# Optimization experiments

Hardware: AMD Instinct MI355X
Metric: run time of the kernel (lower is better)

## Reference

```python
import jax, jax.numpy as jnp
import numpy as np

B, D, K = 8192, 2048, 2048  # batch, input dim, output_dim (must be equal: k==d required by call())


def setup_inputs() -> dict:
    key = jax.random.key(0)
    k1, k2, k3, k4 = jax.random.split(key, 4)
    lim_w = float(np.sqrt(6.0 / (K + D)))        # glorot_uniform for W (k,d)
    lim_v = float(np.sqrt(6.0 / (2 * D + K)))    # glorot_uniform for V (2d,k)
    return {
        "e1": jax.random.normal(k1, (B, D), jnp.float32),
        "e2": jax.random.normal(k2, (B, D), jnp.float32),
        "W": jax.random.uniform(k3, (K, D), jnp.float32, -lim_w, lim_w),
        "V": jax.random.uniform(k4, (2 * D, K), jnp.float32, -lim_v, lim_v),
        "b": jnp.zeros((K,), jnp.float32),
    }


def reference(e1, e2, W, V, b):
    # Faithful translation of the active call() of NeuralTensorDiagLayer.
    # call() tiles flatten(e1) k times and reshapes to (B, d, k); index algebra
    # shows x[p, q, r] = e1[(p*d+q)%B, r] * e2[(p*d+q)%B, r] * W[q, r]
    # (requires k == d for the W broadcast), then mean over the last axis (size k).
    # Equivalent efficient form: u = ((e1*e2) @ W.T)/k, then gather rows (p*d+q)%B.
    bsz, d = e1.shape
    k = W.shape[0]
    ff = jnp.concatenate([e1, e2], axis=-1) @ V              # (B, k) feedforward GEMM
    u = ((e1 * e2) @ W.T) / k                                # (B, k) diag bilinear, mean over k
    cols = jnp.arange(k)[None, :]                            # (1, k)
    rows = (jnp.arange(bsz)[:, None] * d + cols) % bsz       # (B, k) batch-mixing index from tile/reshape
    z = u[rows, cols]                                        # (B, k)
    return jnp.tanh(z + ff + b)
```

## Files before the change

kernel.cpp:

```cpp
#include <hip/hip_runtime.h>
#include <hip/hip_bf16.h>

typedef __bf16 bf16;
typedef bf16 bf16x8 __attribute__((ext_vector_type(8)));
typedef bf16 bf16x4 __attribute__((ext_vector_type(4)));
typedef float f32x4 __attribute__((ext_vector_type(4)));

#define AS1 __attribute__((address_space(1)))
#define AS3 __attribute__((address_space(3)))

__device__ __forceinline__ void gload_lds16(const void* g, void* l) {
    __builtin_amdgcn_global_load_lds((const AS1 void*)g, (AS3 void*)l, 16, 0, 0);
}

__device__ __forceinline__ float tanh_fast(float x) {
    float e = __expf(2.0f * x);
    return fmaf(-2.0f, __builtin_amdgcn_rcpf(e + 1.0f), 1.0f);
}

__global__ __launch_bounds__(256) void conv_fused(
    const float* __restrict__ e1, const float* __restrict__ e2,
    const float* __restrict__ W, const float* __restrict__ V,
    bf16* __restrict__ Xb, bf16* __restrict__ Vt, float* __restrict__ zs)
{
    __shared__ float tile[64][65];
    const int bid = blockIdx.x;
    const int t = threadIdx.x;

    if (bid < 8192) {
        const int r = bid;
        const int c = r & 2047, m = r >> 11;
        const size_t rb = (size_t)r * 2048;

        const float4* p1 = (const float4*)(e1 + rb) + t * 2;
        const float4* p2 = (const float4*)(e2 + rb) + t * 2;
        const float4* pw = (const float4*)(W + (size_t)c * 2048) + t * 2;
        float4 a0 = p1[0], a1 = p1[1];
        float4 b0 = p2[0], b1 = p2[1];
        float4 w0 = pw[0], w1 = pw[1];

        float dot = a0.x*b0.x*w0.x + a0.y*b0.y*w0.y + a0.z*b0.z*w0.z + a0.w*b0.w*w0.w
                  + a1.x*b1.x*w1.x + a1.y*b1.y*w1.y + a1.z*b1.z*w1.z + a1.w*b1.w*w1.w;

        bf16x8 xa, xb;
        xa[0]=(bf16)a0.x; xa[1]=(bf16)a0.y; xa[2]=(bf16)a0.z; xa[3]=(bf16)a0.w;
        xa[4]=(bf16)a1.x; xa[5]=(bf16)a1.y; xa[6]=(bf16)a1.z; xa[7]=(bf16)a1.w;
        xb[0]=(bf16)b0.x; xb[1]=(bf16)b0.y; xb[2]=(bf16)b0.z; xb[3]=(bf16)b0.w;
        xb[4]=(bf16)b1.x; xb[5]=(bf16)b1.y; xb[6]=(bf16)b1.z; xb[7]=(bf16)b1.w;

        *(bf16x8*)(Xb + (size_t)r * 4096 + t * 8)        = xa;
        *(bf16x8*)(Xb + (size_t)r * 4096 + 2048 + t * 8) = xb;

        #pragma unroll
        for (int off = 32; off; off >>= 1) dot += __shfl_xor(dot, off);
        float* red = &tile[0][0];
        if ((t & 63) == 0) red[t >> 6] = dot;
        __syncthreads();
        if (t == 0) zs[m * 2048 + c] = (red[0]+red[1]+red[2]+red[3]) * (1.0f/2048.0f);
    } else {
        const int vb = bid - 8192;
        const int k0 = (vb >> 5) * 64;
        const int c0 = (vb & 31) * 64;
        const int rr = t >> 4;
        const int cc = (t & 15) * 4;

        #pragma unroll
        for (int r4 = 0; r4 < 4; ++r4) {
            int row = r4 * 16 + rr;
            float4 v = *(const float4*)(V + (size_t)(k0 + row) * 2048 + c0 + cc);
            tile[row][cc + 0] = v.x; tile[row][cc + 1] = v.y;
            tile[row][cc + 2] = v.z; tile[row][cc + 3] = v.w;
        }
        __syncthreads();
        #pragma unroll
        for (int r4 = 0; r4 < 4; ++r4) {
            int crow = r4 * 16 + rr;
            bf16x4 o;
            o[0] = (bf16)tile[cc + 0][crow];
            o[1] = (bf16)tile[cc + 1][crow];
            o[2] = (bf16)tile[cc + 2][crow];
            o[3] = (bf16)tile[cc + 3][crow];
            *(bf16x4*)(Vt + (size_t)(c0 + crow) * 4096 + k0 + cc) = o;
        }
    }
}

__global__ __launch_bounds__(512, 2) void gemm_ep(
    const bf16* __restrict__ Xb, const bf16* __restrict__ Vt,
    const float* __restrict__ zs, const float* __restrict__ bias,
    float* __restrict__ out)
{
    extern __shared__ char smem[];
    const int tid  = threadIdx.x;
    const int lane = tid & 63;
    const int wid  = tid >> 6;
    const int wr = wid >> 2, wc = wid & 3;
    const int mtile = blockIdx.x & 31;
    const int ntile = blockIdx.x >> 5;
    const int row0 = mtile * 256, col0 = ntile * 256;

    const int srow = tid >> 3;
    const int scb  = ((tid & 7) * 16) ^ ((srow & 7) << 4);
    const bf16* Abase = Xb + (size_t)(row0 + srow) * 4096 + (scb >> 1);
    const bf16* Bbase = Vt + (size_t)(col0 + srow) * 4096 + (scb >> 1);

    const int lr  = lane & 15;
    const int lkb = (lane >> 4) * 16;

    f32x4 acc[2][2][4][2] = {};
    bf16x8 aA[4][2];
    bf16x8 bB[2][2][2];

    auto stage = [&](int c, int kt) {
        char* Al = smem + c * 65536 + tid * 16;
        char* Bl = smem + c * 65536 + 32768 + tid * 16;
        const bf16* Ag = Abase + (size_t)kt * 64;
        const bf16* Bg = Bbase + (size_t)kt * 64;
        #pragma unroll
        for (int r = 0; r < 4; ++r) gload_lds16(Ag + (size_t)r * 262144, Al + r * 8192);
        #pragma unroll
        for (int r = 0; r < 4; ++r) gload_lds16(Bg + (size_t)r * 262144, Bl + r * 8192);
    };

    auto ldsA = [&](const char* Ab, int qm, int i, int ks) -> bf16x8 {
        const int R = wr * 128 + qm * 64 + i * 16 + lr;
        const int cb = ks * 64 + lkb;
        return *(const bf16x8*)(Ab + R * 128 + (cb ^ ((R & 7) << 4)));
    };
    auto ldsB = [&](const char* Bb, int qn, int j, int ks) -> bf16x8 {
        const int R = wc * 64 + qn * 32 + j * 16 + lr;
        const int cb = ks * 64 + lkb;
        return *(const bf16x8*)(Bb + R * 128 + (cb ^ ((R & 7) << 4)));
    };

    auto window1 = [&](int c) {
        const char* Ab = smem + c * 65536;
        const char* Bb = smem + c * 65536 + 32768;
        #pragma unroll
        for (int i = 0; i < 4; ++i) { aA[i][0] = ldsA(Ab, 0, i, 0); aA[i][1] = ldsA(Ab, 0, i, 1); }
        #pragma unroll
        for (int j = 0; j < 2; ++j) { bB[0][j][0] = ldsB(Bb, 0, j, 0); bB[0][j][1] = ldsB(Bb, 0, j, 1); }
        __builtin_amdgcn_s_setprio(1);
        #pragma unroll
        for (int ks = 0; ks < 2; ++ks)
            #pragma unroll
            for (int i = 0; i < 4; ++i)
                #pragma unroll
                for (int j = 0; j < 2; ++j)
                    acc[0][0][i][j] = __builtin_amdgcn_mfma_f32_16x16x32_bf16(
                        aA[i][ks], bB[0][j][ks], acc[0][0][i][j], 0, 0, 0);
        __builtin_amdgcn_s_setprio(0);
        #pragma unroll
        for (int j = 0; j < 2; ++j) { bB[1][j][0] = ldsB(Bb, 1, j, 0); bB[1][j][1] = ldsB(Bb, 1, j, 1); }
        __builtin_amdgcn_s_setprio(1);
        #pragma unroll
        for (int ks = 0; ks < 2; ++ks)
            #pragma unroll
            for (int i = 0; i < 4; ++i)
                #pragma unroll
                for (int j = 0; j < 2; ++j)
                    acc[0][1][i][j] = __builtin_amdgcn_mfma_f32_16x16x32_bf16(
                        aA[i][ks], bB[1][j][ks], acc[0][1][i][j], 0, 0, 0);
        __builtin_amdgcn_s_setprio(0);
        #pragma unroll
        for (int i = 0; i < 4; ++i) { aA[i][0] = ldsA(Ab, 1, i, 0); aA[i][1] = ldsA(Ab, 1, i, 1); }
        __builtin_amdgcn_s_setprio(1);
        #pragma unroll
        for (int ks = 0; ks < 2; ++ks)
            #pragma unroll
            for (int i = 0; i < 4; ++i)
                #pragma unroll
                for (int j = 0; j < 2; ++j)
                    acc[1][1][i][j] = __builtin_amdgcn_mfma_f32_16x16x32_bf16(
                        aA[i][ks], bB[1][j][ks], acc[1][1][i][j], 0, 0, 0);
        __builtin_amdgcn_s_setprio(0);
    };

    auto mfma_q10 = [&]() {
        __builtin_amdgcn_s_setprio(1);
        #pragma unroll
        for (int ks = 0; ks < 2; ++ks)
            #pragma unroll
            for (int i = 0; i < 4; ++i)
                #pragma unroll
                for (int j = 0; j < 2; ++j)
                    acc[1][0][i][j] = __builtin_amdgcn_mfma_f32_16x16x32_bf16(
                        aA[i][ks], bB[0][j][ks], acc[1][0][i][j], 0, 0, 0);
        __builtin_amdgcn_s_setprio(0);
    };

    stage(0, 0);
    stage(1, 1);
    asm volatile("s_waitcnt vmcnt(8)" ::: "memory");
    __builtin_amdgcn_s_barrier();

    #pragma unroll 2
    for (int t = 0; t < 62; ++t) {
        const int c = t & 1;
        window1(c);
        __builtin_amdgcn_s_barrier();
        stage(c, t + 2);
        mfma_q10();
        asm volatile("s_waitcnt vmcnt(8)" ::: "memory");
        __builtin_amdgcn_s_barrier();
    }
    window1(0);
    __builtin_amdgcn_s_barrier();
    mfma_q10();
    asm volatile("s_waitcnt vmcnt(0)" ::: "memory");
    __builtin_amdgcn_s_barrier();
    window1(1);
    mfma_q10();

    const int lq = lane >> 4;
    float zb[2][2][4];
    #pragma unroll
    for (int qn = 0; qn < 2; ++qn)
        #pragma unroll
        for (int j = 0; j < 2; ++j) {
            const int ccol = col0 + wc * 64 + qn * 32 + j * 16 + lr;
            const float bb = bias[ccol];
            #pragma unroll
            for (int q = 0; q < 4; ++q) zb[qn][j][q] = zs[q * 2048 + ccol] + bb;
        }
    #pragma unroll
    for (int qm = 0; qm < 2; ++qm)
        #pragma unroll
        for (int i = 0; i < 4; ++i)
            #pragma unroll
            for (int q = 0; q < 4; ++q) {
                float* orow = out + (size_t)(row0 + wr * 128 + qm * 64 + i * 16
                                             + lq * 4 + q) * 2048
                                  + col0 + wc * 64 + lr;
                #pragma unroll
                for (int qn = 0; qn < 2; ++qn)
                    #pragma unroll
                    for (int j = 0; j < 2; ++j)
                        orow[qn * 32 + j * 16] =
                            tanh_fast(acc[qm][qn][i][j][q] + zb[qn][j][q]);
            }
}

extern "C" void kernel_launch(void* const* d_in, const int* in_sizes, int n_in,
                              void* d_out, int out_size, void* d_ws, size_t ws_size,
                              hipStream_t stream) {
    const float* e1 = (const float*)d_in[0];
    const float* e2 = (const float*)d_in[1];
    const float* W  = (const float*)d_in[2];
    const float* V  = (const float*)d_in[3];
    const float* b  = (const float*)d_in[4];
    float* out = (float*)d_out;

    char* ws = (char*)d_ws;
    bf16*  Xb = (bf16*)ws;
    bf16*  Vt = (bf16*)(ws + (size_t)64 * 1024 * 1024);
    float* zs = (float*)(ws + (size_t)80 * 1024 * 1024);

    conv_fused<<<10240, 256, 0, stream>>>(e1, e2, W, V, Xb, Vt, zs);

    hipFuncSetAttribute((const void*)gemm_ep,
                        hipFuncAttributeMaxDynamicSharedMemorySize, 131072);
    gemm_ep<<<256, 512, 131072, stream>>>(Xb, Vt, zs, b, out);
}
```

Baseline: 162.4 us.

## Fuse fp32-to-bf16 conversion of activations into the GEMM A-tile loader

The prep kernel no longer writes a bf16 copy of concat(e1,e2) to the workspace. The GEMM now loads fp32 e1/e2 tiles into registers, converts them to bf16 and writes them into swizzled LDS. B tiles still arrive through direct global-to-LDS loads. This removes a large intermediate write and re-read, but it doubles the bytes fetched per A tile, replaces async LDS loads with register-staged ones and adds register pressure under the 512-thread, 2-block launch bound.

```diff
diff --git a/kernel.cpp b/kernel.cpp
--- a/kernel.cpp
+++ b/kernel.cpp
@@ -21,7 +21,7 @@
 __global__ __launch_bounds__(256) void conv_fused(
     const float* __restrict__ e1, const float* __restrict__ e2,
     const float* __restrict__ W, const float* __restrict__ V,
-    bf16* __restrict__ Xb, bf16* __restrict__ Vt, float* __restrict__ zs)
+    bf16* __restrict__ Vt, float* __restrict__ zs)
 {
     __shared__ float tile[64][65];
     const int bid = blockIdx.x;
@@ -41,15 +41,6 @@
 
         float dot = a0.x*b0.x*w0.x + a0.y*b0.y*w0.y + a0.z*b0.z*w0.z + a0.w*b0.w*w0.w
                   + a1.x*b1.x*w1.x + a1.y*b1.y*w1.y + a1.z*b1.z*w1.z + a1.w*b1.w*w1.w;
-
-        bf16x8 xa, xb;
-        xa[0]=(bf16)a0.x; xa[1]=(bf16)a0.y; xa[2]=(bf16)a0.z; xa[3]=(bf16)a0.w;
-        xa[4]=(bf16)a1.x; xa[5]=(bf16)a1.y; xa[6]=(bf16)a1.z; xa[7]=(bf16)a1.w;
-        xb[0]=(bf16)b0.x; xb[1]=(bf16)b0.y; xb[2]=(bf16)b0.z; xb[3]=(bf16)b0.w;
-        xb[4]=(bf16)b1.x; xb[5]=(bf16)b1.y; xb[6]=(bf16)b1.z; xb[7]=(bf16)b1.w;
-
-        *(bf16x8*)(Xb + (size_t)r * 4096 + t * 8)        = xa;
-        *(bf16x8*)(Xb + (size_t)r * 4096 + 2048 + t * 8) = xb;
 
         #pragma unroll
         for (int off = 32; off; off >>= 1) dot += __shfl_xor(dot, off);
@@ -86,9 +77,9 @@
 }
 
 __global__ __launch_bounds__(512, 2) void gemm_ep(
-    const bf16* __restrict__ Xb, const bf16* __restrict__ Vt,
-    const float* __restrict__ zs, const float* __restrict__ bias,
-    float* __restrict__ out)
+    const float* __restrict__ e1, const float* __restrict__ e2,
+    const bf16* __restrict__ Vt, const float* __restrict__ zs,
+    const float* __restrict__ bias, float* __restrict__ out)
 {
     extern __shared__ char smem[];
     const int tid  = threadIdx.x;
@@ -101,7 +92,8 @@
 
     const int srow = tid >> 3;
     const int scb  = ((tid & 7) * 16) ^ ((srow & 7) << 4);
-    const bf16* Abase = Xb + (size_t)(row0 + srow) * 4096 + (scb >> 1);
+    const float* Af1 = e1 + (size_t)(row0 + srow) * 2048 + (scb >> 1);
+    const float* Af2 = e2 + (size_t)(row0 + srow) * 2048 + (scb >> 1);
     const bf16* Bbase = Vt + (size_t)(col0 + srow) * 4096 + (scb >> 1);
 
     const int lr  = lane & 15;
@@ -110,14 +102,30 @@
     f32x4 acc[2][2][4][2] = {};
     bf16x8 aA[4][2];
     bf16x8 bB[2][2][2];
-
-    auto stage = [&](int c, int kt) {
-        char* Al = smem + c * 65536 + tid * 16;
+    float4 f[8];
+
+    auto loadF = [&](int kt) {
+        const float* src = (kt < 32 ? Af1 : Af2) + (size_t)(kt & 31) * 64;
+        #pragma unroll
+        for (int r = 0; r < 4; ++r) {
+            f[2*r]   = *(const float4*)(src + (size_t)r * 131072);
+            f[2*r+1] = *(const float4*)(src + (size_t)r * 131072 + 4);
+        }
+    };
+    auto writeA = [&](int c) {
+        #pragma unroll
+        for (int r = 0; r < 4; ++r) {
+            bf16x8 w;
+            w[0]=(bf16)f[2*r].x;   w[1]=(bf16)f[2*r].y;
+            w[2]=(bf16)f[2*r].z;   w[3]=(bf16)f[2*r].w;
+            w[4]=(bf16)f[2*r+1].x; w[5]=(bf16)f[2*r+1].y;
+            w[6]=(bf16)f[2*r+1].z; w[7]=(bf16)f[2*r+1].w;
+            *(bf16x8*)(smem + c * 65536 + tid * 16 + r * 8192) = w;
+        }
+    };
+    auto stageB = [&](int c, int kt) {
         char* Bl = smem + c * 65536 + 32768 + tid * 16;
-        const bf16* Ag = Abase + (size_t)kt * 64;
         const bf16* Bg = Bbase + (size_t)kt * 64;
-        #pragma unroll
-        for (int r = 0; r < 4; ++r) gload_lds16(Ag + (size_t)r * 262144, Al + r * 8192);
         #pragma unroll
         for (int r = 0; r < 4; ++r) gload_lds16(Bg + (size_t)r * 262144, Bl + r * 8192);
     };
@@ -189,19 +197,23 @@
         __builtin_amdgcn_s_setprio(0);
     };
 
-    stage(0, 0);
-    stage(1, 1);
-    asm volatile("s_waitcnt vmcnt(8)" ::: "memory");
+    loadF(0);  writeA(0);
+    loadF(1);  writeA(1);
+    stageB(0, 0);
+    stageB(1, 1);
+    asm volatile("s_waitcnt vmcnt(0) lgkmcnt(0)" ::: "memory");
     __builtin_amdgcn_s_barrier();
 
     #pragma unroll 2
     for (int t = 0; t < 62; ++t) {
         const int c = t & 1;
+        loadF(t + 2);
         window1(c);
         __builtin_amdgcn_s_barrier();
-        stage(c, t + 2);
+        writeA(c);
+        stageB(c, t + 2);
         mfma_q10();
-        asm volatile("s_waitcnt vmcnt(8)" ::: "memory");
+        asm volatile("s_waitcnt lgkmcnt(0)" ::: "memory");
         __builtin_amdgcn_s_barrier();
     }
     window1(0);
@@ -252,13 +264,12 @@
     float* out = (float*)d_out;
 
     char* ws = (char*)d_ws;
-    bf16*  Xb = (bf16*)ws;
-    bf16*  Vt = (bf16*)(ws + (size_t)64 * 1024 * 1024);
-    float* zs = (float*)(ws + (size_t)80 * 1024 * 1024);
-
-    conv_fused<<<10240, 256, 0, stream>>>(e1, e2, W, V, Xb, Vt, zs);
+    bf16*  Vt = (bf16*)ws;
+    float* zs = (float*)(ws + (size_t)16 * 1024 * 1024);
+
+    conv_fused<<<10240, 256, 0, stream>>>(e1, e2, W, V, Vt, zs);
 
     hipFuncSetAttribute((const void*)gemm_ep,
                         hipFuncAttributeMaxDynamicSharedMemorySize, 131072);
-    gemm_ep<<<256, 512, 131072, stream>>>(Xb, Vt, zs, b, out);
-}
+    gemm_ep<<<256, 512, 131072, stream>>>(e1, e2, Vt, zs, b, out);
+}
```

New measurement: 189.9 us. 1.17x slower.
